# Kernel tuning notes

Hardware: AMD Instinct MI355X
Metric: run time of the kernel (lower is better)

## Reference

```python
import jax, jax.numpy as jnp
from jax import lax
import numpy as np

B, CIN, H, W = 32, 3, 384, 384
CF, HF, WF = 256, 32, 32   # features_map_dimensions; linear_map_dims = (32, 32)
MD = 64                    # metadata_dimension
DN = ('NCHW', 'OIHW', 'NCHW')


def setup_inputs() -> dict:
    key = jax.random.key(0)
    ks = jax.random.split(key, 12)
    n = lambda k, s, sc=1.0: jax.random.normal(k, s, jnp.float32) * sc
    return {
        'inputs': n(ks[0], (B, CIN, H, W)),
        'feature_map_outputs': n(ks[1], (B, CF, HF, WF)),
        'metadata_inputs': n(ks[2], (B, 16, MD)),
        # mapping_conv: Conv2d(CF, 16, 1)
        'mc_w': n(ks[3], (16, CF), 0.05),
        'mc_b': n(ks[4], (16,), 0.05),
        # metadata_linear: Linear(MD, 32*32)
        'ml_w': n(ks[5], (HF * WF, MD), 0.05),
        'ml_b': n(ks[6], (HF * WF,), 0.05),
        # inputs_conv: Conv2d(CIN, 4, 3)
        'ic_w': n(ks[7], (4, CIN, 3, 3), 0.1),
        'ic_b': n(ks[8], (4,), 0.1),
        # bboxes_layer: Conv2d(4, 4, (HF, WF))
        'bb_w': n(ks[9], (4, 4, HF, WF), 0.02),
        'bb_b': n(ks[10], (4,), 0.02),
    }


def _pad_hw(x):
    # torch ZeroPad2d((pr//2, pr-pr//2, pc//2, pc-pc//2)) with pr=HF-1 (width), pc=WF-1 (height)
    pr, pc = HF - 1, WF - 1
    return jnp.pad(x, ((0, 0), (0, 0), (pc // 2, pc - pc // 2), (pr // 2, pr - pr // 2)))


def reference(inputs, feature_map_outputs, metadata_inputs,
              mc_w, mc_b, ml_w, ml_b, ic_w, ic_b, bb_w, bb_b):
    b = inputs.shape[0]
    # 1x1 conv over feature map: [B,CF,HF,WF] -> [B,16,HF,WF]
    convolved_feats = jnp.einsum('bchw,oc->bohw', feature_map_outputs, mc_w) + mc_b[None, :, None, None]
    # metadata linear: [B,16,MD] -> [B,16,HF,WF]
    meta_feats = (metadata_inputs @ ml_w.T + ml_b).reshape(b, 16, HF, WF)
    # batched matmul over last two dims: [B,16,HF,WF] @ [B,16,HF(WF),WF]
    linear_feats = jnp.einsum('bkij,bkjl->bkil', convolved_feats, meta_feats)
    # inputs conv (valid 3x3) -> zero-pad 1 -> sigmoid (note: sigmoid AFTER pad, borders = 0.5)
    ci = lax.conv_general_dilated(inputs, ic_w, (1, 1), 'VALID', dimension_numbers=DN) + ic_b[None, :, None, None]
    ci = jax.nn.sigmoid(jnp.pad(ci, ((0, 0), (0, 0), (1, 1), (1, 1))))  # [B,4,H,W]
    # per-sample dynamic conv weights: sigmoid(linear_feats) -> [B,4,4,HF,WF]
    wts = jax.nn.sigmoid(linear_feats).reshape(b, 4, 4, HF, WF)

    def per_sample(x, w):  # x: [4,H,W], w: [4,4,HF,WF]
        return lax.conv_general_dilated(x[None], w, (1, 1), 'VALID', dimension_numbers=DN)[0]

    mapped = jax.vmap(per_sample)(ci, wts)        # [B,4,H-HF+1,W-WF+1]
    mapped = _pad_hw(mapped)                      # [B,4,H,W]
    out = lax.conv_general_dilated(mapped, bb_w, (1, 1), 'VALID', dimension_numbers=DN) + bb_b[None, :, None, None]
    return _pad_hw(out)                           # [B,4,H,W]
```

## Files before the change

### kernel.cpp

```cpp
#include <hip/hip_runtime.h>
#include <hip/hip_bf16.h>

typedef __hip_bfloat16 bf16;
typedef __attribute__((ext_vector_type(8))) short short8_t;
typedef __attribute__((ext_vector_type(16))) float f32x16;
typedef __attribute__((ext_vector_type(2))) unsigned int uint2v;

#define HH 384
#define HW (384*384)
#define TOT_ELEMS (32u*4u*147456u)

__device__ inline float b2f(bf16 v){ return __bfloat162float(v); }
__device__ inline bf16  f2b(float v){ return __float2bfloat16(v); }
__device__ inline float sigm(float x){ return 1.f/(1.f+__expf(-x)); }

__device__ inline uint ab2(uint h, uint l){ return __builtin_amdgcn_alignbyte(h, l, 2); }

__device__ inline short8_t mk8p(uint2v a, uint2v b){
    union { uint u[4]; short8_t s; } t;
    t.u[0]=a[0]; t.u[1]=a[1]; t.u[2]=b[0]; t.u[3]=b[1]; return t.s;
}

__global__ __launch_bounds__(256) void ci_kernel(const float* __restrict__ in,
                                                 const float* __restrict__ icw,
                                                 const float* __restrict__ icb,
                                                 bf16* __restrict__ ci)
{
    __shared__ float sw[108];
    __shared__ float sb[4];
    int tid = threadIdx.x;
    if (tid < 108) sw[tid] = icw[tid];
    if (tid < 4)   sb[tid] = icb[tid];
    __syncthreads();
    size_t idx = (size_t)blockIdx.x * 256 + tid;
    int x = (int)(idx % HH);
    int y = (int)((idx / HH) % HH);
    int b = (int)(idx / ((size_t)HH * HH));
    float v[4];
    if (y > 0 && y < HH-1 && x > 0 && x < HH-1) {
        float a0 = sb[0], a1 = sb[1], a2 = sb[2], a3 = sb[3];
        for (int ic = 0; ic < 3; ic++) {
            #pragma unroll
            for (int dy = 0; dy < 3; dy++) {
                #pragma unroll
                for (int dx = 0; dx < 3; dx++) {
                    float iv = in[((size_t)(b*3+ic)*HH + (y-1+dy))*HH + (x-1+dx)];
                    a0 = fmaf(iv, sw[0*27 + ic*9 + dy*3 + dx], a0);
                    a1 = fmaf(iv, sw[1*27 + ic*9 + dy*3 + dx], a1);
                    a2 = fmaf(iv, sw[2*27 + ic*9 + dy*3 + dx], a2);
                    a3 = fmaf(iv, sw[3*27 + ic*9 + dy*3 + dx], a3);
                }
            }
        }
        v[0]=sigm(a0); v[1]=sigm(a1); v[2]=sigm(a2); v[3]=sigm(a3);
    } else {
        v[0]=v[1]=v[2]=v[3]=0.5f;
    }
    #pragma unroll
    for (int o = 0; o < 4; o++)
        ci[((size_t)(b*4+o)*HH + y)*HH + x] = f2b(v[o]);
}

__global__ __launch_bounds__(256) void convfeats_kernel(const float* __restrict__ fm,
                                                        const float* __restrict__ mcw,
                                                        const float* __restrict__ mcb,
                                                        float* __restrict__ cf)
{
    __shared__ float sw[256*16];
    int tid = threadIdx.x;
    int b = blockIdx.x >> 2, chunk = blockIdx.x & 3;
    for (int i = tid; i < 4096; i += 256) {
        int k = i / 256, c = i % 256;
        sw[c*16 + k] = mcw[k*256 + c];
    }
    __syncthreads();
    int hw = chunk*256 + tid;
    float acc[16];
    #pragma unroll
    for (int k = 0; k < 16; k++) acc[k] = mcb[k];
    const float* f = fm + (size_t)b*256*1024 + hw;
    for (int c = 0; c < 256; c++) {
        float v = f[(size_t)c*1024];
        const float4* wp = (const float4*)(sw + c*16);
        #pragma unroll
        for (int q = 0; q < 4; q++) {
            float4 t = wp[q];
            acc[q*4+0] = fmaf(v, t.x, acc[q*4+0]);
            acc[q*4+1] = fmaf(v, t.y, acc[q*4+1]);
            acc[q*4+2] = fmaf(v, t.z, acc[q*4+2]);
            acc[q*4+3] = fmaf(v, t.w, acc[q*4+3]);
        }
    }
    #pragma unroll
    for (int k = 0; k < 16; k++)
        cf[(size_t)b*16384 + k*1024 + hw] = acc[k];
}

__global__ __launch_bounds__(256) void wts_kernel(const float* __restrict__ meta,
                                                  const float* __restrict__ mlw,
                                                  const float* __restrict__ mlb,
                                                  const float* __restrict__ cf,
                                                  bf16* __restrict__ wout)
{
    __shared__ float sm[64];
    __shared__ float sA[1024];
    __shared__ float sB[1024];
    int tid = threadIdx.x;
    int b = blockIdx.x >> 4, k = blockIdx.x & 15;
    if (tid < 64) sm[tid] = meta[(size_t)b*16*64 + k*64 + tid];
    #pragma unroll
    for (int q = 0; q < 4; q++)
        sA[q*256 + tid] = cf[(size_t)b*16384 + k*1024 + q*256 + tid];
    __syncthreads();
    #pragma unroll
    for (int q = 0; q < 4; q++) {
        int hw = q*256 + tid;
        const float4* wr = (const float4*)(mlw + (size_t)hw*64);
        float a = mlb[hw];
        #pragma unroll
        for (int d4 = 0; d4 < 16; d4++) {
            float4 t = wr[d4];
            a = fmaf(t.x, sm[d4*4+0], a);
            a = fmaf(t.y, sm[d4*4+1], a);
            a = fmaf(t.z, sm[d4*4+2], a);
            a = fmaf(t.w, sm[d4*4+3], a);
        }
        sB[hw] = a;
    }
    __syncthreads();
    #pragma unroll
    for (int q = 0; q < 4; q++) {
        int il = q*256 + tid;
        int i = il >> 5, l = il & 31;
        float a = 0.f;
        #pragma unroll
        for (int j = 0; j < 32; j++)
            a = fmaf(sA[i*32 + j], sB[j*32 + l], a);
        wout[(size_t)b*16384 + k*1024 + il] = f2b(sigm(a));
    }
}

__global__ __launch_bounds__(256) void atab1F_kernel(const ushort* __restrict__ wts,
                                                     ushort* __restrict__ out)
{
    int g = blockIdx.x*256 + threadIdx.x;
    int lane = g & 63, half = (g >> 6) & 1;
    int rest = g >> 7;
    int kyp = rest % 39; int rest2 = rest / 39;
    int c = rest2 & 3, b = rest2 >> 2;
    int r = lane & 31, hi = lane >> 5;
    int dyA = r >> 2, mA = r & 3;
    int ch = mA*4 + c, ky = kyp - dyA, kx = 16*half + 8*hi;
    ushort v[8];
    if (ky >= 0 && ky < 32) {
        const ushort* src = wts + ((size_t)b*16 + ch)*1024 + ky*32 + kx;
        #pragma unroll
        for (int i=0;i<8;i++) v[i] = src[i];
    } else {
        #pragma unroll
        for (int i=0;i<8;i++) v[i] = 0;
    }
    __builtin_memcpy(out + (size_t)g*8, v, 16);
}

__global__ __launch_bounds__(256) void atab2F_kernel(const float* __restrict__ bbw,
                                                     ushort* __restrict__ out)
{
    int g = blockIdx.x*256 + threadIdx.x;
    int lane = g & 63, half = (g >> 6) & 1;
    int rest = g >> 7;
    int kyp = rest % 39;
    int c = rest / 39;
    int r = lane & 31, hi = lane >> 5;
    int dyA = r >> 2, mA = r & 3;
    int ch = mA*4 + c, ky = kyp - dyA, kx = 16*half + 8*hi;
    ushort v[8];
    if (ky >= 0 && ky < 32) {
        const float* src = bbw + (size_t)ch*1024 + ky*32 + kx;
        #pragma unroll
        for (int i=0;i<8;i++) { bf16 t = f2b(src[i]); v[i] = *(ushort*)&t; }
    } else {
        #pragma unroll
        for (int i=0;i<8;i++) v[i] = 0;
    }
    __builtin_memcpy(out + (size_t)g*8, v, 16);
}

#define G_LOADX4(dst, addr, OFF) \
    asm volatile("global_load_dwordx4 %0, %1, off offset:" OFF : "=v"(dst) : "v"(addr))

#define ISSUE_A(A0_, A1_, ap_, e_)                                   \
{                                                                    \
    const ushort* p_ = (ap_) + (unsigned)(e_)*1024u;                 \
    G_LOADX4(A0_, p_, "0");                                          \
    G_LOADX4(A1_, p_, "1024");                                       \
}

#define ISSUE_B8(S, ADDR)                                                    \
    asm volatile(                                                            \
        "ds_read2_b32 %0, %8 offset0:0 offset1:1\n\t"                        \
        "ds_read2_b32 %1, %8 offset0:2 offset1:3\n\t"                        \
        "ds_read2_b32 %2, %8 offset0:8 offset1:9\n\t"                        \
        "ds_read2_b32 %3, %8 offset0:10 offset1:11\n\t"                      \
        "ds_read2_b32 %4, %8 offset0:16 offset1:17\n\t"                      \
        "ds_read2_b32 %5, %8 offset0:18 offset1:19\n\t"                      \
        "ds_read2_b32 %6, %8 offset0:24 offset1:25\n\t"                      \
        "ds_read2_b32 %7, %8 offset0:26 offset1:27"                          \
        : "=v"(S[0]), "=v"(S[1]), "=v"(S[2]), "=v"(S[3]), "=v"(S[4]),        \
          "=v"(S[5]), "=v"(S[6]), "=v"(S[7])                                 \
        : "v"(ADDR) : "memory")

#define KWAIT(VN, LN) do {                                                      \
    asm volatile("s_waitcnt vmcnt(" VN ") lgkmcnt(" LN ")" ::: "memory");       \
    __builtin_amdgcn_sched_barrier(0); } while (0)

#define MMp(acc_, A_, Pa, Pb) \
    acc_ = __builtin_amdgcn_mfma_f32_32x32x16_bf16(A_, mk8p(Pa, Pb), acc_, 0, 0, 0)

#define STEP1B(S, A0_, A1_, VN, LN) { KWAIT(VN, LN);                          \
    MMp(q0, A0_, S[0], S[1]);  MMp(q1, A0_, S[4], S[5]);                      \
    MMp(q0, A1_, S[2], S[3]);  MMp(q1, A1_, S[6], S[7]); }

#define STEP2B(S, C0_, C1_, VN, LN) { KWAIT(VN, LN);                          \
    MMp(u0, C0_, S[0], S[1]);  MMp(u1, C0_, S[4], S[5]);                      \
    MMp(u0, C1_, S[2], S[3]);  MMp(u1, C1_, S[6], S[7]); }

#define STEP12B(S, A0_, A1_, C0_, C1_, VN, LN) { KWAIT(VN, LN);               \
    MMp(q0, A0_, S[0], S[1]);   MMp(u0, C0_, S[0], S[1]);                     \
    MMp(q1, A0_, S[4], S[5]);   MMp(u1, C0_, S[4], S[5]);                     \
    MMp(q0, A1_, S[2], S[3]);   MMp(u0, C1_, S[2], S[3]);                     \
    MMp(q1, A1_, S[6], S[7]);   MMp(u1, C1_, S[6], S[7]); }

template<bool PER_B, bool OUT_BF16, bool ADD_BIAS>
__global__ __launch_bounds__(256, 3) void conv32_duo(const ushort* __restrict__ in,
                                                     const ushort* __restrict__ atabF,
                                                     const float* __restrict__ bias,
                                                     void* __restrict__ outp)
{
    __shared__ uint sbuf[63*160];

    int d = blockIdx.x;
    int L = (d & 7) * 144 + (d >> 3);
    int b = L / 36; int rem = L % 36;
    int yb = rem / 3, xb = rem % 3;
    int yv = yb * 32;
    int x0 = xb * 128;

    int tid = threadIdx.x;
    int l = tid & 63, w = tid >> 6;
    int rg = (w >> 1) * 16;
    int xs = (w & 1) * 64;
    int hi = l >> 5;

    int s = xs + (l & 31) + 8*hi;
    int p = s & 1;
    const uint* swl = sbuf + (unsigned)(rg*160) + (unsigned)(p*80 + ((s - p) >> 1));
    uint baddr0 = (uint)(size_t)(const void*)swl;

    f32x16 q0, q1, u0, u1;
    #pragma unroll
    for (int i = 0; i < 16; i++) { q0[i]=0.f; q1[i]=0.f; u0[i]=0.f; u1[i]=0.f; }

    unsigned chbase0 = (unsigned)b*589824u + (unsigned)yv*384u + (unsigned)x0;

    for (int c = 0; c < 4; ++c) {
        if (c) __syncthreads();
        unsigned chb = chbase0 + (unsigned)c*147456u;
        for (int qq = tid; qq < 1260; qq += 256) {
            int row = qq / 20, k = qq - row*20;
            unsigned gi = chb + (unsigned)row*384u + (unsigned)k*8u;
            if (gi > TOT_ELEMS - 16u) gi = TOT_ELEMS - 16u;
            const uint* gp = (const uint*)(in + gi);
            uint d0 = gp[0], d1 = gp[1], d2 = gp[2], d3 = gp[3], d4 = gp[4];
            unsigned widx = (unsigned)row*160u + (unsigned)k*4u;
            uint4* w0 = (uint4*)&sbuf[widx];
            uint4* w1 = (uint4*)&sbuf[widx + 80u];
            *w0 = make_uint4(d0, d1, d2, d3);
            *w1 = make_uint4(ab2(d1,d0), ab2(d2,d1), ab2(d3,d2), ab2(d4,d3));
        }
        __syncthreads();

        const ushort* ap1 = atabF + (size_t)((PER_B ? (b*4 + c) : c) * 39) * 1024 + l*8;
        short8_t xA0, xA1, yA0, yA1;
        short8_t x20, x21, y20, y21;
        uint2v sE[8], sO[8];
        uint baddr = baddr0;

        ISSUE_B8(sE, baddr); baddr += 640u;
        ISSUE_A(xA0, xA1, ap1, 0);

        ISSUE_B8(sO, baddr); baddr += 640u;
        ISSUE_A(yA0, yA1, ap1, 1);
        STEP1B(sE, xA0, xA1, "2", "8");
        ISSUE_B8(sE, baddr); baddr += 640u;
        ISSUE_A(xA0, xA1, ap1, 2);
        STEP1B(sO, yA0, yA1, "2", "8");
        ISSUE_B8(sO, baddr); baddr += 640u;
        ISSUE_A(yA0, yA1, ap1, 3);
        STEP1B(sE, xA0, xA1, "2", "8");
        ISSUE_B8(sE, baddr); baddr += 640u;
        ISSUE_A(xA0, xA1, ap1, 4);
        STEP1B(sO, yA0, yA1, "2", "8");
        ISSUE_B8(sO, baddr); baddr += 640u;
        ISSUE_A(yA0, yA1, ap1, 5);
        STEP1B(sE, xA0, xA1, "2", "8");
        ISSUE_B8(sE, baddr); baddr += 640u;
        ISSUE_A(xA0, xA1, ap1, 6);
        STEP1B(sO, yA0, yA1, "2", "8");
        ISSUE_B8(sO, baddr); baddr += 640u;
        ISSUE_A(yA0, yA1, ap1, 7);
        STEP1B(sE, xA0, xA1, "2", "8");
        ISSUE_B8(sE, baddr); baddr += 640u;
        ISSUE_A(xA0, xA1, ap1, 8);
        ISSUE_A(x20, x21, ap1, 0);
        STEP1B(sO, yA0, yA1, "4", "8");

        #pragma unroll 1
        for (int t = 0; t < 15; ++t) {
            int r = 8 + 2*t;
            ISSUE_B8(sO, baddr); baddr += 640u;
            ISSUE_A(yA0, yA1, ap1, r+1); ISSUE_A(y20, y21, ap1, r-7);
            STEP12B(sE, xA0, xA1, x20, x21, "4", "8");
            ISSUE_B8(sE, baddr); baddr += 640u;
            ISSUE_A(xA0, xA1, ap1, r+2); ISSUE_A(x20, x21, ap1, r-6);
            STEP12B(sO, yA0, yA1, y20, y21, "4", "8");
        }
        ISSUE_B8(sO, baddr); baddr += 640u;
        ISSUE_A(y20, y21, ap1, 31);
        STEP12B(sE, xA0, xA1, x20, x21, "2", "8");

        ISSUE_B8(sE, baddr); baddr += 640u; ISSUE_A(x20, x21, ap1, 32); STEP2B(sO, y20, y21, "2", "8");
        ISSUE_B8(sO, baddr); baddr += 640u; ISSUE_A(y20, y21, ap1, 33); STEP2B(sE, x20, x21, "2", "8");
        ISSUE_B8(sE, baddr); baddr += 640u; ISSUE_A(x20, x21, ap1, 34); STEP2B(sO, y20, y21, "2", "8");
        ISSUE_B8(sO, baddr); baddr += 640u; ISSUE_A(y20, y21, ap1, 35); STEP2B(sE, x20, x21, "2", "8");
        ISSUE_B8(sE, baddr); baddr += 640u; ISSUE_A(x20, x21, ap1, 36); STEP2B(sO, y20, y21, "2", "8");
        ISSUE_B8(sO, baddr); baddr += 640u; ISSUE_A(y20, y21, ap1, 37); STEP2B(sE, x20, x21, "2", "8");
        ISSUE_B8(sE, baddr); baddr += 640u; ISSUE_A(x20, x21, ap1, 38); STEP2B(sO, y20, y21, "2", "8");
        STEP2B(sE, x20, x21, "0", "0");
    }

    float bv0 = 0.f, bv1 = 0.f, bv2 = 0.f, bv3 = 0.f;
    if (ADD_BIAS) { bv0 = bias[0]; bv1 = bias[1]; bv2 = bias[2]; bv3 = bias[3]; }

    #pragma unroll
    for (int j = 0; j < 2; j++) {
        int ox = x0 + xs + 32*j + (l & 31);
        if (ox > 352) continue;
        int px = ox + 15;
        #pragma unroll
        for (int rgi = 0; rgi < 16; rgi++) {
            int m  = rgi & 3;
            int dy = 2*(rgi >> 2) + hi;
            float v1 = (j == 0 ? q0[rgi] : q1[rgi]);
            float v2 = (j == 0 ? u0[rgi] : u1[rgi]);
            float bb = (m == 0 ? bv0 : m == 1 ? bv1 : m == 2 ? bv2 : bv3);
            int oy1 = yv + rg + dy;
            if (oy1 <= 352) {
                size_t o = ((size_t)(b*4 + m))*HW + (size_t)(oy1 + 15)*HH + px;
                float v = v1 + (ADD_BIAS ? bb : 0.f);
                if constexpr (OUT_BF16) ((bf16*)outp)[o] = f2b(v);
                else                    ((float*)outp)[o] = v;
            }
            int oy2 = yv + rg + 8 + dy;
            if (oy2 <= 352) {
                size_t o = ((size_t)(b*4 + m))*HW + (size_t)(oy2 + 15)*HH + px;
                float v = v2 + (ADD_BIAS ? bb : 0.f);
                if constexpr (OUT_BF16) ((bf16*)outp)[o] = f2b(v);
                else                    ((float*)outp)[o] = v;
            }
        }
    }
}

extern "C" void kernel_launch(void* const* d_in, const int* in_sizes, int n_in,
                              void* d_out, int out_size, void* d_ws, size_t ws_size,
                              hipStream_t stream)
{
    const float* inputs = (const float*)d_in[0];
    const float* fm     = (const float*)d_in[1];
    const float* meta   = (const float*)d_in[2];
    const float* mcw    = (const float*)d_in[3];
    const float* mcb    = (const float*)d_in[4];
    const float* mlw    = (const float*)d_in[5];
    const float* mlb    = (const float*)d_in[6];
    const float* icw    = (const float*)d_in[7];
    const float* icb    = (const float*)d_in[8];
    const float* bbw    = (const float*)d_in[9];
    const float* bbb    = (const float*)d_in[10];

    char* ws = (char*)d_ws;
    bf16*   ci     = (bf16*) ws;
    bf16*   mapped = (bf16*)(ws + 37748736);
    float*  cf     = (float*)(ws + 75497472);
    bf16*   wts    = (bf16*)(ws + 77594624);
    ushort* atab1F = (ushort*)(ws + 78643200);
    ushort* atab2F = (ushort*)(ws + 88866816);

    ci_kernel<<<18432, 256, 0, stream>>>(inputs, icw, icb, ci);
    convfeats_kernel<<<128, 256, 0, stream>>>(fm, mcw, mcb, cf);
    wts_kernel<<<512, 256, 0, stream>>>(meta, mlw, mlb, cf, wts);
    atab1F_kernel<<<2496, 256, 0, stream>>>((const ushort*)wts, atab1F);
    atab2F_kernel<<<78, 256, 0, stream>>>(bbw, atab2F);

    hipMemsetAsync(mapped, 0, 37748736, stream);
    conv32_duo<true, true, false><<<1152, 256, 0, stream>>>(
        (const ushort*)ci, atab1F, nullptr, mapped);

    hipMemsetAsync(d_out, 0, (size_t)out_size * 4, stream);
    conv32_duo<false, false, true><<<1152, 256, 0, stream>>>(
        (const ushort*)mapped, atab2F, bbb, d_out);
}
```

Baseline: 446.7 us.

## Zero only border regions and split feature 1x1 conv across channel halves

Full-buffer memsets of the mapped intermediate and the output are replaced by small kernels that zero only the padded border pixels, which the conv kernels never write. The 1x1 feature conv is split into two channel halves to double the block count, and the partial sums plus bias are added in wts_kernel. A full wait on outstanding memory counters is added at the end of each channel loop. The partial buffer reuses the mapped region, which is safe only because mapped is written after wts_kernel has consumed it.

New measurement: 412.6 us. -7.6%, faster.

```diff
diff --git a/kernel.cpp b/kernel.cpp
--- a/kernel.cpp
+++ b/kernel.cpp
@@ -9,6 +9,7 @@
 #define HH 384
 #define HW (384*384)
 #define TOT_ELEMS (32u*4u*147456u)
+#define NBORD 22847
 
 __device__ inline float b2f(bf16 v){ return __bfloat162float(v); }
 __device__ inline bf16  f2b(float v){ return __float2bfloat16(v); }
@@ -61,27 +62,29 @@
         ci[((size_t)(b*4+o)*HH + y)*HH + x] = f2b(v[o]);
 }
 
-__global__ __launch_bounds__(256) void convfeats_kernel(const float* __restrict__ fm,
-                                                        const float* __restrict__ mcw,
-                                                        const float* __restrict__ mcb,
-                                                        float* __restrict__ cf)
-{
-    __shared__ float sw[256*16];
+__global__ __launch_bounds__(256) void convfeats_part_kernel(const float* __restrict__ fm,
+                                                             const float* __restrict__ mcw,
+                                                             float* __restrict__ part)
+{
+    __shared__ float sw[128*16];
     int tid = threadIdx.x;
-    int b = blockIdx.x >> 2, chunk = blockIdx.x & 3;
-    for (int i = tid; i < 4096; i += 256) {
-        int k = i / 256, c = i % 256;
-        sw[c*16 + k] = mcw[k*256 + c];
+    int bx = blockIdx.x;
+    int b = bx >> 3;
+    int rem = bx & 7;
+    int chunk = rem >> 1, half = rem & 1;
+    for (int i = tid; i < 2048; i += 256) {
+        int k = i >> 7, cl = i & 127;
+        sw[cl*16 + k] = mcw[k*256 + half*128 + cl];
     }
     __syncthreads();
     int hw = chunk*256 + tid;
     float acc[16];
     #pragma unroll
-    for (int k = 0; k < 16; k++) acc[k] = mcb[k];
-    const float* f = fm + (size_t)b*256*1024 + hw;
-    for (int c = 0; c < 256; c++) {
-        float v = f[(size_t)c*1024];
-        const float4* wp = (const float4*)(sw + c*16);
+    for (int k = 0; k < 16; k++) acc[k] = 0.f;
+    const float* f = fm + (size_t)b*256*1024 + (size_t)(half*128)*1024 + hw;
+    for (int cl = 0; cl < 128; cl++) {
+        float v = f[(size_t)cl*1024];
+        const float4* wp = (const float4*)(sw + cl*16);
         #pragma unroll
         for (int q = 0; q < 4; q++) {
             float4 t = wp[q];
@@ -93,13 +96,14 @@
     }
     #pragma unroll
     for (int k = 0; k < 16; k++)
-        cf[(size_t)b*16384 + k*1024 + hw] = acc[k];
+        part[(size_t)(b*2 + half)*16384 + k*1024 + hw] = acc[k];
 }
 
 __global__ __launch_bounds__(256) void wts_kernel(const float* __restrict__ meta,
                                                   const float* __restrict__ mlw,
                                                   const float* __restrict__ mlb,
-                                                  const float* __restrict__ cf,
+                                                  const float* __restrict__ part,
+                                                  const float* __restrict__ mcb,
                                                   bf16* __restrict__ wout)
 {
     __shared__ float sm[64];
@@ -108,9 +112,13 @@
     int tid = threadIdx.x;
     int b = blockIdx.x >> 4, k = blockIdx.x & 15;
     if (tid < 64) sm[tid] = meta[(size_t)b*16*64 + k*64 + tid];
-    #pragma unroll
-    for (int q = 0; q < 4; q++)
-        sA[q*256 + tid] = cf[(size_t)b*16384 + k*1024 + q*256 + tid];
+    float bk = mcb[k];
+    #pragma unroll
+    for (int q = 0; q < 4; q++) {
+        int hw = q*256 + tid;
+        sA[hw] = part[(size_t)(b*2 + 0)*16384 + k*1024 + hw]
+               + part[(size_t)(b*2 + 1)*16384 + k*1024 + hw] + bk;
+    }
     __syncthreads();
     #pragma unroll
     for (int q = 0; q < 4; q++) {
@@ -184,6 +192,28 @@
         for (int i=0;i<8;i++) v[i] = 0;
     }
     __builtin_memcpy(out + (size_t)g*8, v, 16);
+}
+
+__global__ __launch_bounds__(256) void bz16_kernel(ushort* __restrict__ out)
+{
+    int g = blockIdx.x*256 + threadIdx.x;
+    if (g >= NBORD*128) return;
+    int i = g % NBORD, bc = g / NBORD;
+    int y, x;
+    if (i < 11904) { int r = i / 384; y = (r < 15) ? r : 353 + r; x = i % 384; }
+    else { int j = i - 11904; y = 15 + j / 31; int cc = j % 31; x = (cc < 15) ? cc : 353 + cc; }
+    out[(size_t)bc*HW + (size_t)y*HH + x] = 0;
+}
+
+__global__ __launch_bounds__(256) void bz32_kernel(float* __restrict__ out)
+{
+    int g = blockIdx.x*256 + threadIdx.x;
+    if (g >= NBORD*128) return;
+    int i = g % NBORD, bc = g / NBORD;
+    int y, x;
+    if (i < 11904) { int r = i / 384; y = (r < 15) ? r : 353 + r; x = i % 384; }
+    else { int j = i - 11904; y = 15 + j / 31; int cc = j % 31; x = (cc < 15) ? cc : 353 + cc; }
+    out[(size_t)bc*HW + (size_t)y*HH + x] = 0.f;
 }
 
 #define G_LOADX4(dst, addr, OFF) \
@@ -281,8 +311,8 @@
         __syncthreads();
 
         const ushort* ap1 = atabF + (size_t)((PER_B ? (b*4 + c) : c) * 39) * 1024 + l*8;
-        short8_t xA0, xA1, yA0, yA1;
-        short8_t x20, x21, y20, y21;
+        short8_t xA0, xA1, x20, x21;
+        short8_t yA0, yA1, y20, y21;
         uint2v sE[8], sO[8];
         uint baddr = baddr0;
 
@@ -337,6 +367,8 @@
         ISSUE_B8(sO, baddr); baddr += 640u; ISSUE_A(y20, y21, ap1, 37); STEP2B(sE, x20, x21, "2", "8");
         ISSUE_B8(sE, baddr); baddr += 640u; ISSUE_A(x20, x21, ap1, 38); STEP2B(sO, y20, y21, "2", "8");
         STEP2B(sE, x20, x21, "0", "0");
+
+        asm volatile("s_waitcnt vmcnt(0) lgkmcnt(0)" ::: "memory");
     }
 
     float bv0 = 0.f, bv1 = 0.f, bv2 = 0.f, bv3 = 0.f;
@@ -391,22 +423,22 @@
     char* ws = (char*)d_ws;
     bf16*   ci     = (bf16*) ws;
     bf16*   mapped = (bf16*)(ws + 37748736);
-    float*  cf     = (float*)(ws + 75497472);
+    float*  part   = (float*)(ws + 37748736);
     bf16*   wts    = (bf16*)(ws + 77594624);
     ushort* atab1F = (ushort*)(ws + 78643200);
     ushort* atab2F = (ushort*)(ws + 88866816);
 
     ci_kernel<<<18432, 256, 0, stream>>>(inputs, icw, icb, ci);
-    convfeats_kernel<<<128, 256, 0, stream>>>(fm, mcw, mcb, cf);
-    wts_kernel<<<512, 256, 0, stream>>>(meta, mlw, mlb, cf, wts);
+    convfeats_part_kernel<<<256, 256, 0, stream>>>(fm, mcw, part);
+    wts_kernel<<<512, 256, 0, stream>>>(meta, mlw, mlb, part, mcb, wts);
     atab1F_kernel<<<2496, 256, 0, stream>>>((const ushort*)wts, atab1F);
     atab2F_kernel<<<78, 256, 0, stream>>>(bbw, atab2F);
 
-    hipMemsetAsync(mapped, 0, 37748736, stream);
+    bz16_kernel<<<11424, 256, 0, stream>>>((ushort*)mapped);
     conv32_duo<true, true, false><<<1152, 256, 0, stream>>>(
         (const ushort*)ci, atab1F, nullptr, mapped);
 
-    hipMemsetAsync(d_out, 0, (size_t)out_size * 4, stream);
+    bz32_kernel<<<11424, 256, 0, stream>>>((float*)d_out);
     conv32_duo<false, false, true><<<1152, 256, 0, stream>>>(
         (const ushort*)mapped, atab2F, bbb, d_out);
 }
```
